# Kernel tuning notes

Measured on AMD Instinct MI355X. Metric: run time of the kernel, lower is better.

Reference implementation:

```python
import jax, jax.numpy as jnp
import numpy as np

B, S, H = 8, 8192, 128          # batch, num_cities, hidden_size
SSIZE, DSIZE = 2, 1             # static (x,y) feats, dynamic feats
STEPS = 20                      # station_num_lim (decode length)


def setup_inputs() -> dict:
    key = jax.random.key(0)
    ks = jax.random.split(key, 16)
    sc = 0.05
    inp = {
        'static': jax.random.normal(ks[0], (B, SSIZE, S), jnp.float32),
        'dynamic': jnp.zeros((B, DSIZE, S), jnp.float32),
        # Encoder convs (kernel_size=1 -> plain linear over channel dim)
        'W_s': jax.random.normal(ks[1], (H, SSIZE), jnp.float32) * sc,
        'b_s': jnp.zeros((H,), jnp.float32),
        'W_d': jax.random.normal(ks[2], (H, DSIZE), jnp.float32) * sc,
        'b_d': jnp.zeros((H,), jnp.float32),
        'W_dec': jax.random.normal(ks[3], (H, SSIZE), jnp.float32) * sc,
        'b_dec': jnp.zeros((H,), jnp.float32),
        # LSTMCell
        'W_ih': jax.random.normal(ks[4], (4 * H, H), jnp.float32) * sc,
        'W_hh': jax.random.normal(ks[5], (4 * H, H), jnp.float32) * sc,
        'b_ih': jnp.zeros((4 * H,), jnp.float32),
        'b_hh': jnp.zeros((4 * H,), jnp.float32),
        # Pointer projections
        'W_ref': jax.random.normal(ks[6], (H, H), jnp.float32) * sc,
        'b_ref': jnp.zeros((H,), jnp.float32),
        'W_pd': jax.random.normal(ks[7], (H, H), jnp.float32) * sc,
        'b_pd': jnp.zeros((H,), jnp.float32),
        'W_q': jax.random.normal(ks[8], (H, H), jnp.float32) * sc,
        'b_q': jnp.zeros((H,), jnp.float32),
        # Additive attention vector (Attention.W, shape (1,H) in torch)
        'W_att': jax.random.normal(ks[9], (H,), jnp.float32) * sc,
        'station_num_lim': STEPS,
    }
    return inp


def reference(static, dynamic, W_s, b_s, W_d, b_d, W_dec, b_dec,
              W_ih, W_hh, b_ih, b_hh, W_ref, b_ref, W_pd, b_pd,
              W_q, b_q, W_att, station_num_lim):
    Bb, _, Ss = static.shape
    Hh = W_s.shape[0]

    # static/dynamic encoders: Conv1d(k=1) == channelwise linear
    static_h = jnp.einsum('bis,hi->bhs', static, W_s) + b_s[None, :, None]
    dynamic_h = jnp.einsum('bis,hi->bhs', dynamic, W_d) + b_d[None, :, None]
    mask = jnp.ones((Bb, Ss), static.dtype)

    def lstm_cell(x, h, c):
        gates = x @ W_ih.T + b_ih + h @ W_hh.T + b_hh
        i, f, g, o = jnp.split(gates, 4, axis=1)
        c2 = jax.nn.sigmoid(f) * c + jax.nn.sigmoid(i) * jnp.tanh(g)
        h2 = jax.nn.sigmoid(o) * jnp.tanh(c2)
        return h2, c2

    def step(carry, _):
        dec_in, hh, cc = carry                      # dec_in: (B, SSIZE)
        dec_hidden = dec_in @ W_dec.T + b_dec       # decoder Encoder, (B, H)
        hh, cc = lstm_cell(dec_hidden, hh, cc)
        # per-step projections (as in the original Pointer.forward)
        ref = jnp.einsum('bhs,gh->bgs', static_h, W_ref) + b_ref[None, :, None]
        dyn = jnp.einsum('bhs,gh->bgs', dynamic_h, W_pd) + b_pd[None, :, None]
        q = hh @ W_q.T + b_q                        # (B, H)
        hidden = jnp.tanh(q[:, :, None] + ref + dyn)  # (B, H, S)
        attns = jnp.einsum('h,bhs->bs', W_att, hidden)
        probs = jax.nn.softmax(attns + mask * 10000.0, axis=1)
        prob = jnp.max(probs, axis=1)               # greedy (eval) select
        ptr = jnp.argmax(probs, axis=1)
        logp = jnp.log(prob)
        dec_in2 = jnp.take_along_axis(static, ptr[:, None, None], axis=2)[:, :, 0]
        return (dec_in2, hh, cc), (ptr, logp)

    dec0 = jnp.zeros((Bb, static.shape[1]), static.dtype)   # x0
    hh0 = jnp.zeros((Bb, Hh), static.dtype)
    cc0 = jnp.zeros((Bb, Hh), static.dtype)
    _, (tour_idx, tour_logp) = jax.lax.scan(
        step, (dec0, hh0, cc0), None, length=station_num_lim)
    return tour_idx.T, tour_logp.T                  # (B, steps), (B, steps)
```

## Files before the change

### kernel.cpp

```cpp
#include <hip/hip_runtime.h>
#include <hip/hip_bf16.h>


#define SS 8192
#define HH 128
#define NB 8

constexpr float kLog2e  = 1.4426950408889634f;
constexpr float kLn2    = 0.6931471805599453f;
constexpr float kBucket = 9.765625e-4f;
constexpr float kBL2e   = kLog2e * 9.765625e-4f;

__device__ __forceinline__ float fsig(float x) {
  return __builtin_amdgcn_rcpf(1.0f + __builtin_amdgcn_exp2f(-x * kLog2e));
}
__device__ __forceinline__ float ftanh(float x) {
  float z = __builtin_amdgcn_exp2f(x * (2.0f * kLog2e));
  return fmaf(-2.0f, __builtin_amdgcn_rcpf(z + 1.0f), 1.0f);
}

__device__ __forceinline__ unsigned long long cld64(const unsigned long long* p) {
  return __hip_atomic_load(p, __ATOMIC_RELAXED, __HIP_MEMORY_SCOPE_AGENT);
}
__device__ __forceinline__ void cst64(unsigned long long* p, unsigned long long v) {
  __hip_atomic_store(p, v, __ATOMIC_RELAXED, __HIP_MEMORY_SCOPE_AGENT);
}

__global__ __launch_bounds__(256, 1)
void drl4_kernel(const float* __restrict__ g_static,
                 const float* __restrict__ g_dynamic,
                 const float* __restrict__ W_s,  const float* __restrict__ b_s,
                 const float* __restrict__ W_d,  const float* __restrict__ b_d,
                 const float* __restrict__ W_dec,const float* __restrict__ b_dec,
                 const float* __restrict__ W_ih, const float* __restrict__ W_hh,
                 const float* __restrict__ b_ih, const float* __restrict__ b_hh,
                 const float* __restrict__ W_ref,const float* __restrict__ b_ref,
                 const float* __restrict__ W_pd, const float* __restrict__ b_pd,
                 const float* __restrict__ W_q,  const float* __restrict__ b_q,
                 const float* __restrict__ W_att,const int* __restrict__ steps_p,
                 float* __restrict__ out,
                 unsigned long long* __restrict__ wrec,
                 unsigned long long* __restrict__ hhrec) {
  const int tid = threadIdx.x;
  const int bid = blockIdx.x;
  const int b   = bid >> 5;
  const int blk = bid & 31;
  const int steps = *steps_p;

  __shared__ float4 s_pack[128];
  __shared__ float  s_ebias[128];
  __shared__ float  s_gb[512];
  __shared__ float  s_g1x[512];
  __shared__ float  s_g1y[512];
  __shared__ float  s_h[128];
  __shared__ __align__(16) float s_qe[128];
  __shared__ float  s_scr[256];

  const int city = blk * 256 + tid;
  const float sx = g_static[(b * 2 + 0) * SS + city];
  const float sy = g_static[(b * 2 + 1) * SS + city];
  const float dd = g_dynamic[b * SS + city];

  const int qrow  = (tid >> 6) * 32 + (tid & 31);
  const int qhalf = (tid >> 5) & 1;
  float wq[64];
  {
    const float* p = W_q + qrow * HH + qhalf * 64;
    #pragma unroll
    for (int j = 0; j < 64; j += 4) {
      float4 v = *(const float4*)(p + j);
      wq[j] = v.x; wq[j+1] = v.y; wq[j+2] = v.z; wq[j+3] = v.w;
    }
  }
  const int ho = tid & 15, hk = tid >> 4;
  float whh[8];
  {
    const float* p = W_hh + (blk * 16 + ho) * HH + hk * 8;
    #pragma unroll
    for (int j = 0; j < 8; j += 4) {
      float4 v = *(const float4*)(p + j);
      whh[j] = v.x; whh[j+1] = v.y; whh[j+2] = v.z; whh[j+3] = v.w;
    }
  }

  for (int g = tid; g < 512; g += 256) {
    const float* wr = W_ih + g * HH;
    float acc = b_ih[g] + b_hh[g];
    float ax = 0.f, ay = 0.f;
    for (int k = 0; k < HH; ++k) {
      float w = wr[k];
      acc = fmaf(w, b_dec[k],      acc);
      ax  = fmaf(w, W_dec[2*k],    ax);
      ay  = fmaf(w, W_dec[2*k+1],  ay);
    }
    s_gb[g] = acc; s_g1x[g] = ax; s_g1y[g] = ay;
  }
  if (tid < 128) {
    float a0 = 0.f, a1 = 0.f, c0 = 0.f, e1 = 0.f, e2 = 0.f;
    const float* wr = W_ref + tid * HH;
    const float* wp = W_pd  + tid * HH;
    for (int k = 0; k < HH; ++k) {
      float w = wr[k], v = wp[k];
      a0 = fmaf(w, W_s[2 * k],     a0);
      a1 = fmaf(w, W_s[2 * k + 1], a1);
      e1 = fmaf(w, b_s[k],         e1);
      c0 = fmaf(v, W_d[k],         c0);
      e2 = fmaf(v, b_d[k],         e2);
    }
    const float sc = 2.0f * kLog2e;
    s_pack[tid]  = make_float4(a0 * sc, a1 * sc, c0 * sc, W_att[tid]);
    s_ebias[tid] = e1 + e2 + b_ref[tid] + b_pd[tid] + b_q[tid];
  }
  float cstate = 0.0f;
  __syncthreads();

  float zb[128], watt[128];
  #pragma unroll
  for (int h = 0; h < 128; ++h) {
    float4 p = s_pack[h];
    zb[h]   = __builtin_amdgcn_exp2f(fmaf(p.x, sx, fmaf(p.y, sy, p.z * dd)));
    watt[h] = p.w;
  }

  const int wv = tid >> 6;
  const int ln = tid & 63;
  for (int t = 0; t < steps; ++t) {
    float hp0 = 0.f, hp1 = 0.f, hp2 = 0.f, hp3 = 0.f;
    float selx = 0.f, sely = 0.f;
    if (t > 0) {
      if (tid < 128) {
        const unsigned expect = (unsigned)t;
        const unsigned long long* wp = wrec + ((t - 1) * 8 + b) * 128;
        const unsigned long long* hp = hhrec + (t & 1) * 4096 + b * 512 + tid;
        unsigned long long w0, w1, h0, h1, h2, h3;
        for (;;) {
          w0 = cld64(wp + ln);       w1 = cld64(wp + 64 + ln);
          h0 = cld64(hp);            h1 = cld64(hp + 128);
          h2 = cld64(hp + 256);      h3 = cld64(hp + 384);
          if (((unsigned)w0 >> 27) == expect && ((unsigned)w1 >> 27) == expect &&
              (unsigned)(h0 >> 32) == expect && (unsigned)(h1 >> 32) == expect &&
              (unsigned)(h2 >> 32) == expect && (unsigned)(h3 >> 32) == expect)
            break;
          __builtin_amdgcn_s_sleep(1);
        }
        unsigned k0 = (unsigned)w0 & 0x07FFFFFFu;
        unsigned k1 = (unsigned)w1 & 0x07FFFFFFu;
        unsigned wmax = k0 > k1 ? k0 : k1;
        #pragma unroll
        for (int k = 1; k < 64; k <<= 1) {
          unsigned o = __shfl_xor(wmax, k);
          wmax = wmax > o ? wmax : o;
        }
        const int ix = 8191 - (int)(wmax & 0x1FFFu);
        hp0 = __uint_as_float((unsigned)h0);
        hp1 = __uint_as_float((unsigned)h1);
        hp2 = __uint_as_float((unsigned)h2);
        hp3 = __uint_as_float((unsigned)h3);
        selx = g_static[(b * 2 + 0) * SS + ix];
        sely = g_static[(b * 2 + 1) * SS + ix];
      }
    }
    if (tid < 128) {
      float gi, gf, gg, go;
      if (t == 0) {
        gi = s_gb[tid];       gf = s_gb[tid + 128];
        gg = s_gb[tid + 256]; go = s_gb[tid + 384];
      } else {
        gi = fmaf(selx, s_g1x[tid],     fmaf(sely, s_g1y[tid],     s_gb[tid]     + hp0));
        gf = fmaf(selx, s_g1x[tid+128], fmaf(sely, s_g1y[tid+128], s_gb[tid+128] + hp1));
        gg = fmaf(selx, s_g1x[tid+256], fmaf(sely, s_g1y[tid+256], s_gb[tid+256] + hp2));
        go = fmaf(selx, s_g1x[tid+384], fmaf(sely, s_g1y[tid+384], s_gb[tid+384] + hp3));
      }
      cstate  = fmaf(fsig(gf), cstate, fsig(gi) * ftanh(gg));
      s_h[tid] = fsig(go) * ftanh(cstate);
    }
    __syncthreads();
    {
      const float* hs = s_h + (qhalf << 6);
      float qa = 0.f;
      #pragma unroll
      for (int u = 0; u < 64; ++u) qa = fmaf(wq[u], hs[u], qa);
      float qo = __shfl_xor(qa, 32);
      if (qhalf == 0) {
        float qe = (qa + qo + s_ebias[qrow]) * (2.0f * kLog2e);
        s_qe[qrow] = __builtin_amdgcn_exp2f(qe);
      }
    }
    {
      const float* hs2 = s_h + hk * 8;
      float pa = 0.f;
      #pragma unroll
      for (int u = 0; u < 8; ++u) pa = fmaf(whh[u], hs2[u], pa);
      s_scr[tid] = pa;
    }
    __syncthreads();
    if (tid < 16) {
      float acc = 0.f;
      #pragma unroll
      for (int j = 0; j < 16; ++j) acc += s_scr[j * 16 + tid];
      cst64(hhrec + ((t + 1) & 1) * 4096 + b * 512 + blk * 16 + tid,
            ((unsigned long long)(unsigned)(t + 1) << 32) |
                __float_as_uint(acc));
    }
    float a0 = 0.f, a1 = 0.f, a2 = 0.f, a3 = 0.f;
    #pragma unroll
    for (int h = 0; h < 128; h += 4) {
      float4 zq = *(const float4*)(s_qe + h);
      float z0 = zb[h+0] * zq.x, z1 = zb[h+1] * zq.y;
      float z2 = zb[h+2] * zq.z, z3 = zb[h+3] * zq.w;
      float r0 = __builtin_amdgcn_rcpf(z0 + 1.0f);
      float r1 = __builtin_amdgcn_rcpf(z1 + 1.0f);
      float r2 = __builtin_amdgcn_rcpf(z2 + 1.0f);
      float r3 = __builtin_amdgcn_rcpf(z3 + 1.0f);
      a0 = fmaf(watt[h+0], fmaf(-2.0f, r0, 1.0f), a0);
      a1 = fmaf(watt[h+1], fmaf(-2.0f, r1, 1.0f), a1);
      a2 = fmaf(watt[h+2], fmaf(-2.0f, r2, 1.0f), a2);
      a3 = fmaf(watt[h+3], fmaf(-2.0f, r3, 1.0f), a3);
    }
    float aq = ((a0 + a1) + (a2 + a3)) + 10000.0f;
    int kk = (int)((aq - 10000.0f) * 1024.0f);
    kk = kk < -8192 ? -8192 : (kk > 8191 ? 8191 : kk);
    unsigned key = ((unsigned)(kk + 8192) << 13) | (unsigned)(8191 - city);
    unsigned wmax = key;
    #pragma unroll
    for (int k = 1; k < 64; k <<= 1) {
      unsigned o = __shfl_xor(wmax, k);
      wmax = wmax > o ? wmax : o;
    }
    float m_w = fmaf((float)((int)((wmax >> 13) & 0x3FFFu) - 8192), kBucket,
                     10000.0f);
    float ee = __builtin_amdgcn_exp2f((aq - m_w) * kLog2e);
    #pragma unroll
    for (int k = 1; k < 64; k <<= 1) ee += __shfl_xor(ee, k);
    if (ln == 0)
      cst64(wrec + (t * 8 + b) * 128 + blk * 4 + wv,
            ((unsigned long long)__float_as_uint(ee) << 32) |
                ((unsigned)(t + 1) << 27) | wmax);
  }
  if (blk == 0) {
    for (int s = wv; s < steps; s += 4) {
      const unsigned long long* wp = wrec + (s * 8 + b) * 128;
      const unsigned expect = (unsigned)(s + 1);
      unsigned long long r0, r1;
      for (;;) {
        r0 = cld64(wp + ln); r1 = cld64(wp + 64 + ln);
        if (((unsigned)r0 >> 27) == expect && ((unsigned)r1 >> 27) == expect)
          break;
        __builtin_amdgcn_s_sleep(1);
      }
      unsigned k0 = (unsigned)r0 & 0x07FFFFFFu;
      unsigned k1 = (unsigned)r1 & 0x07FFFFFFu;
      unsigned wmax = k0 > k1 ? k0 : k1;
      #pragma unroll
      for (int k = 1; k < 64; k <<= 1) {
        unsigned o = __shfl_xor(wmax, k);
        wmax = wmax > o ? wmax : o;
      }
      int K  = (int)((wmax >> 13) & 0x3FFFu) - 8192;
      int i0 = (int)((k0 >> 13) & 0x3FFFu) - 8192;
      int i1 = (int)((k1 >> 13) & 0x3FFFu) - 8192;
      float e0 = __uint_as_float((unsigned)(r0 >> 32));
      float e1 = __uint_as_float((unsigned)(r1 >> 32));
      float term = fmaf(e0, __builtin_amdgcn_exp2f((float)(i0 - K) * kBL2e),
                        e1 * __builtin_amdgcn_exp2f((float)(i1 - K) * kBL2e));
      #pragma unroll
      for (int k = 1; k < 64; k <<= 1) term += __shfl_xor(term, k);
      if (ln == 0) {
        out[b * steps + s] = (float)(8191 - (int)(wmax & 0x1FFFu));
        out[NB * steps + b * steps + s] =
            -__builtin_amdgcn_logf(term) * kLn2;
      }
    }
  }
}

extern "C" void kernel_launch(void* const* d_in, const int* in_sizes, int n_in,
                              void* d_out, int out_size, void* d_ws, size_t ws_size,
                              hipStream_t stream) {
  unsigned long long* wrec  = (unsigned long long*)d_ws;
  unsigned long long* hhrec = (unsigned long long*)((char*)d_ws + 163840);
  drl4_kernel<<<dim3(256), dim3(256), 0, stream>>>(
      (const float*)d_in[0],  (const float*)d_in[1],
      (const float*)d_in[2],  (const float*)d_in[3],
      (const float*)d_in[4],  (const float*)d_in[5],
      (const float*)d_in[6],  (const float*)d_in[7],
      (const float*)d_in[8],  (const float*)d_in[9],
      (const float*)d_in[10], (const float*)d_in[11],
      (const float*)d_in[12], (const float*)d_in[13],
      (const float*)d_in[14], (const float*)d_in[15],
      (const float*)d_in[16], (const float*)d_in[17],
      (const float*)d_in[18], (const int*)d_in[19],
      (float*)d_out, wrec, hhrec);
}
```

Before: 225.4 us.

## Add fast-path sc0 L2 mailbox and per-block argmax key for cross-block step sync

The per-step cross-block exchange is restructured. Each block now reduces its four wave keys to one block key through shared memory, so the critical-path poll reads one record per block instead of two per lane-pair. Key and hidden-state records are written twice, once with sc0 stores to a fast copy and once with agent-scope atomics to a fallback copy. Pollers spin on the fast copy with inline-asm sc0 loads and check the fallback every fourth iteration. Block-to-batch mapping is also interleaved (b = bid & 7). The added block barrier and the non-coherent fast path add risk: a missed update can only be recovered through the slower fallback reads.

```diff
diff --git a/kernel.cpp b/kernel.cpp
--- a/kernel.cpp
+++ b/kernel.cpp
@@ -24,6 +24,10 @@
 }
 __device__ __forceinline__ void cst64(unsigned long long* p, unsigned long long v) {
   __hip_atomic_store(p, v, __ATOMIC_RELAXED, __HIP_MEMORY_SCOPE_AGENT);
+}
+__device__ __forceinline__ void l2st64(unsigned long long* p, unsigned long long v) {
+  asm volatile("global_store_dwordx2 %0, %1, off sc0" :: "v"(p), "v"(v)
+               : "memory");
 }
 
 __global__ __launch_bounds__(256, 1)
@@ -39,12 +43,15 @@
                  const float* __restrict__ W_q,  const float* __restrict__ b_q,
                  const float* __restrict__ W_att,const int* __restrict__ steps_p,
                  float* __restrict__ out,
-                 unsigned long long* __restrict__ wrec,
-                 unsigned long long* __restrict__ hhrec) {
+                 unsigned long long* __restrict__ krecA,
+                 unsigned long long* __restrict__ krecF,
+                 unsigned long long* __restrict__ hhA,
+                 unsigned long long* __restrict__ hhF,
+                 unsigned long long* __restrict__ frec) {
   const int tid = threadIdx.x;
   const int bid = blockIdx.x;
-  const int b   = bid >> 5;
-  const int blk = bid & 31;
+  const int b   = bid & 7;
+  const int blk = bid >> 3;
   const int steps = *steps_p;
 
   __shared__ float4 s_pack[128];
@@ -55,6 +62,7 @@
   __shared__ float  s_h[128];
   __shared__ __align__(16) float s_qe[128];
   __shared__ float  s_scr[256];
+  __shared__ unsigned s_wk[4];
 
   const int city = blk * 256 + tid;
   const float sx = g_static[(b * 2 + 0) * SS + city];
@@ -130,22 +138,44 @@
     if (t > 0) {
       if (tid < 128) {
         const unsigned expect = (unsigned)t;
-        const unsigned long long* wp = wrec + ((t - 1) * 8 + b) * 128;
-        const unsigned long long* hp = hhrec + (t & 1) * 4096 + b * 512 + tid;
-        unsigned long long w0, w1, h0, h1, h2, h3;
+        const int kbase = ((t - 1) & 1) * 256 + b * 32 + (tid & 31);
+        const int hbase = (t & 1) * 4096 + b * 512 + tid;
+        const unsigned long long* kF = krecF + kbase;
+        const unsigned long long* hF = hhF + hbase;
+        const unsigned long long* kA = krecA + kbase;
+        const unsigned long long* hA = hhA + hbase;
+        unsigned long long kv, h0, h1, h2, h3;
+        int it = 0;
         for (;;) {
-          w0 = cld64(wp + ln);       w1 = cld64(wp + 64 + ln);
-          h0 = cld64(hp);            h1 = cld64(hp + 128);
-          h2 = cld64(hp + 256);      h3 = cld64(hp + 384);
-          if (((unsigned)w0 >> 27) == expect && ((unsigned)w1 >> 27) == expect &&
-              (unsigned)(h0 >> 32) == expect && (unsigned)(h1 >> 32) == expect &&
-              (unsigned)(h2 >> 32) == expect && (unsigned)(h3 >> 32) == expect)
-            break;
+          unsigned long long fa, f0, f1, f2, f3;
+          asm volatile(
+              "global_load_dwordx2 %0, %5, off sc0\n\t"
+              "global_load_dwordx2 %1, %6, off sc0\n\t"
+              "global_load_dwordx2 %2, %7, off sc0\n\t"
+              "global_load_dwordx2 %3, %8, off sc0\n\t"
+              "global_load_dwordx2 %4, %9, off sc0\n\t"
+              "s_waitcnt vmcnt(0)"
+              : "=v"(fa), "=v"(f0), "=v"(f1), "=v"(f2), "=v"(f3)
+              : "v"(kF), "v"(hF), "v"(hF + 128), "v"(hF + 256), "v"(hF + 384)
+              : "memory");
+          if ((unsigned)(fa >> 32) == expect && (unsigned)(f0 >> 32) == expect &&
+              (unsigned)(f1 >> 32) == expect && (unsigned)(f2 >> 32) == expect &&
+              (unsigned)(f3 >> 32) == expect) {
+            kv = fa; h0 = f0; h1 = f1; h2 = f2; h3 = f3; break;
+          }
+          if ((++it & 3) == 0) {
+            fa = cld64(kA);
+            f0 = cld64(hA);       f1 = cld64(hA + 128);
+            f2 = cld64(hA + 256); f3 = cld64(hA + 384);
+            if ((unsigned)(fa >> 32) == expect && (unsigned)(f0 >> 32) == expect &&
+                (unsigned)(f1 >> 32) == expect && (unsigned)(f2 >> 32) == expect &&
+                (unsigned)(f3 >> 32) == expect) {
+              kv = fa; h0 = f0; h1 = f1; h2 = f2; h3 = f3; break;
+            }
+          }
           __builtin_amdgcn_s_sleep(1);
         }
-        unsigned k0 = (unsigned)w0 & 0x07FFFFFFu;
-        unsigned k1 = (unsigned)w1 & 0x07FFFFFFu;
-        unsigned wmax = k0 > k1 ? k0 : k1;
+        unsigned wmax = (unsigned)kv;
         #pragma unroll
         for (int k = 1; k < 64; k <<= 1) {
           unsigned o = __shfl_xor(wmax, k);
@@ -198,9 +228,11 @@
       float acc = 0.f;
       #pragma unroll
       for (int j = 0; j < 16; ++j) acc += s_scr[j * 16 + tid];
-      cst64(hhrec + ((t + 1) & 1) * 4096 + b * 512 + blk * 16 + tid,
-            ((unsigned long long)(unsigned)(t + 1) << 32) |
-                __float_as_uint(acc));
+      const int hidx = ((t + 1) & 1) * 4096 + b * 512 + blk * 16 + tid;
+      unsigned long long hv =
+          ((unsigned long long)(unsigned)(t + 1) << 32) | __float_as_uint(acc);
+      l2st64(hhF + hidx, hv);
+      cst64(hhA + hidx, hv);
     }
     float a0 = 0.f, a1 = 0.f, a2 = 0.f, a3 = 0.f;
     #pragma unroll
@@ -227,19 +259,32 @@
       unsigned o = __shfl_xor(wmax, k);
       wmax = wmax > o ? wmax : o;
     }
-    float m_w = fmaf((float)((int)((wmax >> 13) & 0x3FFFu) - 8192), kBucket,
-                     10000.0f);
-    float ee = __builtin_amdgcn_exp2f((aq - m_w) * kLog2e);
+    if (ln == 0) s_wk[wv] = wmax;
+    __syncthreads();
+    unsigned bkey = s_wk[0];
+    bkey = bkey > s_wk[1] ? bkey : s_wk[1];
+    bkey = bkey > s_wk[2] ? bkey : s_wk[2];
+    bkey = bkey > s_wk[3] ? bkey : s_wk[3];
+    if (tid == 0) {
+      const int kidx = (t & 1) * 256 + b * 32 + blk;
+      unsigned long long rv =
+          ((unsigned long long)(unsigned)(t + 1) << 32) | bkey;
+      l2st64(krecF + kidx, rv);
+      cst64(krecA + kidx, rv);
+    }
+    float m = fmaf((float)((int)((bkey >> 13) & 0x3FFFu) - 8192), kBucket,
+                   10000.0f);
+    float ee = __builtin_amdgcn_exp2f((aq - m) * kLog2e);
     #pragma unroll
     for (int k = 1; k < 64; k <<= 1) ee += __shfl_xor(ee, k);
     if (ln == 0)
-      cst64(wrec + (t * 8 + b) * 128 + blk * 4 + wv,
+      cst64(frec + (t * 8 + b) * 128 + blk * 4 + wv,
             ((unsigned long long)__float_as_uint(ee) << 32) |
-                ((unsigned)(t + 1) << 27) | wmax);
+                ((unsigned)(t + 1) << 27) | bkey);
   }
   if (blk == 0) {
     for (int s = wv; s < steps; s += 4) {
-      const unsigned long long* wp = wrec + (s * 8 + b) * 128;
+      const unsigned long long* wp = frec + (s * 8 + b) * 128;
       const unsigned expect = (unsigned)(s + 1);
       unsigned long long r0, r1;
       for (;;) {
@@ -277,8 +322,12 @@
 extern "C" void kernel_launch(void* const* d_in, const int* in_sizes, int n_in,
                               void* d_out, int out_size, void* d_ws, size_t ws_size,
                               hipStream_t stream) {
-  unsigned long long* wrec  = (unsigned long long*)d_ws;
-  unsigned long long* hhrec = (unsigned long long*)((char*)d_ws + 163840);
+  char* ws = (char*)d_ws;
+  unsigned long long* krecA = (unsigned long long*)(ws);
+  unsigned long long* krecF = (unsigned long long*)(ws + 4096);
+  unsigned long long* hhA   = (unsigned long long*)(ws + 8192);
+  unsigned long long* hhF   = (unsigned long long*)(ws + 73728);
+  unsigned long long* frec  = (unsigned long long*)(ws + 139264);
   drl4_kernel<<<dim3(256), dim3(256), 0, stream>>>(
       (const float*)d_in[0],  (const float*)d_in[1],
       (const float*)d_in[2],  (const float*)d_in[3],
@@ -290,5 +339,5 @@
       (const float*)d_in[14], (const float*)d_in[15],
       (const float*)d_in[16], (const float*)d_in[17],
       (const float*)d_in[18], (const int*)d_in[19],
-      (float*)d_out, wrec, hhrec);
-}
+      (float*)d_out, krecA, krecF, hhA, hhF, frec);
+}
```

Result: faster. 216.7 us (-3.8%).

## Publish argmax key before softmax sum to shorten cross-block critical path

Applied to the files above, without the earlier changes.

Splits the per-wave record into an early argmax-key record (double-buffered by step parity), written right after the max reduction, and a later full record holding the exp-sum used only by the final log-prob pass. Blocks waiting for the next step now poll the key record, so the exp and sum reduction no longer sit on the inter-step dependency chain. Also vectorises the setup dot-product loops with float4 loads. This adds an extra global store per wave per step and depends on the parity-based buffer reuse being safe across steps.

```diff
diff --git a/kernel.cpp b/kernel.cpp
--- a/kernel.cpp
+++ b/kernel.cpp
@@ -39,8 +39,9 @@
                  const float* __restrict__ W_q,  const float* __restrict__ b_q,
                  const float* __restrict__ W_att,const int* __restrict__ steps_p,
                  float* __restrict__ out,
-                 unsigned long long* __restrict__ wrec,
-                 unsigned long long* __restrict__ hhrec) {
+                 unsigned long long* __restrict__ krec,
+                 unsigned long long* __restrict__ hhrec,
+                 unsigned long long* __restrict__ frec) {
   const int tid = threadIdx.x;
   const int bid = blockIdx.x;
   const int b   = bid >> 5;
@@ -87,11 +88,15 @@
     const float* wr = W_ih + g * HH;
     float acc = b_ih[g] + b_hh[g];
     float ax = 0.f, ay = 0.f;
-    for (int k = 0; k < HH; ++k) {
-      float w = wr[k];
-      acc = fmaf(w, b_dec[k],      acc);
-      ax  = fmaf(w, W_dec[2*k],    ax);
-      ay  = fmaf(w, W_dec[2*k+1],  ay);
+    for (int k = 0; k < HH; k += 4) {
+      float4 w  = *(const float4*)(wr + k);
+      float4 bd = *(const float4*)(b_dec + k);
+      float4 d0 = *(const float4*)(W_dec + 2 * k);
+      float4 d1 = *(const float4*)(W_dec + 2 * k + 4);
+      acc = fmaf(w.x, bd.x, acc); ax = fmaf(w.x, d0.x, ax); ay = fmaf(w.x, d0.y, ay);
+      acc = fmaf(w.y, bd.y, acc); ax = fmaf(w.y, d0.z, ax); ay = fmaf(w.y, d0.w, ay);
+      acc = fmaf(w.z, bd.z, acc); ax = fmaf(w.z, d1.x, ax); ay = fmaf(w.z, d1.y, ay);
+      acc = fmaf(w.w, bd.w, acc); ax = fmaf(w.w, d1.z, ax); ay = fmaf(w.w, d1.w, ay);
     }
     s_gb[g] = acc; s_g1x[g] = ax; s_g1y[g] = ay;
   }
@@ -99,13 +104,22 @@
     float a0 = 0.f, a1 = 0.f, c0 = 0.f, e1 = 0.f, e2 = 0.f;
     const float* wr = W_ref + tid * HH;
     const float* wp = W_pd  + tid * HH;
-    for (int k = 0; k < HH; ++k) {
-      float w = wr[k], v = wp[k];
-      a0 = fmaf(w, W_s[2 * k],     a0);
-      a1 = fmaf(w, W_s[2 * k + 1], a1);
-      e1 = fmaf(w, b_s[k],         e1);
-      c0 = fmaf(v, W_d[k],         c0);
-      e2 = fmaf(v, b_d[k],         e2);
+    for (int k = 0; k < HH; k += 4) {
+      float4 w  = *(const float4*)(wr + k);
+      float4 v  = *(const float4*)(wp + k);
+      float4 s0 = *(const float4*)(W_s + 2 * k);
+      float4 s1 = *(const float4*)(W_s + 2 * k + 4);
+      float4 bs = *(const float4*)(b_s + k);
+      float4 wd = *(const float4*)(W_d + k);
+      float4 bd = *(const float4*)(b_d + k);
+      a0 = fmaf(w.x, s0.x, a0); a1 = fmaf(w.x, s0.y, a1); e1 = fmaf(w.x, bs.x, e1);
+      c0 = fmaf(v.x, wd.x, c0); e2 = fmaf(v.x, bd.x, e2);
+      a0 = fmaf(w.y, s0.z, a0); a1 = fmaf(w.y, s0.w, a1); e1 = fmaf(w.y, bs.y, e1);
+      c0 = fmaf(v.y, wd.y, c0); e2 = fmaf(v.y, bd.y, e2);
+      a0 = fmaf(w.z, s1.x, a0); a1 = fmaf(w.z, s1.y, a1); e1 = fmaf(w.z, bs.z, e1);
+      c0 = fmaf(v.z, wd.z, c0); e2 = fmaf(v.z, bd.z, e2);
+      a0 = fmaf(w.w, s1.z, a0); a1 = fmaf(w.w, s1.w, a1); e1 = fmaf(w.w, bs.w, e1);
+      c0 = fmaf(v.w, wd.w, c0); e2 = fmaf(v.w, bd.w, e2);
     }
     const float sc = 2.0f * kLog2e;
     s_pack[tid]  = make_float4(a0 * sc, a1 * sc, c0 * sc, W_att[tid]);
@@ -130,22 +144,22 @@
     if (t > 0) {
       if (tid < 128) {
         const unsigned expect = (unsigned)t;
-        const unsigned long long* wp = wrec + ((t - 1) * 8 + b) * 128;
+        const unsigned long long* kp =
+            krec + ((t - 1) & 1) * 1024 + b * 128;
         const unsigned long long* hp = hhrec + (t & 1) * 4096 + b * 512 + tid;
-        unsigned long long w0, w1, h0, h1, h2, h3;
+        unsigned long long k0, k1, h0, h1, h2, h3;
         for (;;) {
-          w0 = cld64(wp + ln);       w1 = cld64(wp + 64 + ln);
+          k0 = cld64(kp + ln);       k1 = cld64(kp + 64 + ln);
           h0 = cld64(hp);            h1 = cld64(hp + 128);
           h2 = cld64(hp + 256);      h3 = cld64(hp + 384);
-          if (((unsigned)w0 >> 27) == expect && ((unsigned)w1 >> 27) == expect &&
+          if ((unsigned)(k0 >> 32) == expect && (unsigned)(k1 >> 32) == expect &&
               (unsigned)(h0 >> 32) == expect && (unsigned)(h1 >> 32) == expect &&
               (unsigned)(h2 >> 32) == expect && (unsigned)(h3 >> 32) == expect)
             break;
           __builtin_amdgcn_s_sleep(1);
         }
-        unsigned k0 = (unsigned)w0 & 0x07FFFFFFu;
-        unsigned k1 = (unsigned)w1 & 0x07FFFFFFu;
-        unsigned wmax = k0 > k1 ? k0 : k1;
+        unsigned u0 = (unsigned)k0, u1 = (unsigned)k1;
+        unsigned wmax = u0 > u1 ? u0 : u1;
         #pragma unroll
         for (int k = 1; k < 64; k <<= 1) {
           unsigned o = __shfl_xor(wmax, k);
@@ -227,19 +241,22 @@
       unsigned o = __shfl_xor(wmax, k);
       wmax = wmax > o ? wmax : o;
     }
+    if (ln == 0)
+      cst64(krec + (t & 1) * 1024 + b * 128 + blk * 4 + wv,
+            ((unsigned long long)(unsigned)(t + 1) << 32) | wmax);
     float m_w = fmaf((float)((int)((wmax >> 13) & 0x3FFFu) - 8192), kBucket,
                      10000.0f);
     float ee = __builtin_amdgcn_exp2f((aq - m_w) * kLog2e);
     #pragma unroll
     for (int k = 1; k < 64; k <<= 1) ee += __shfl_xor(ee, k);
     if (ln == 0)
-      cst64(wrec + (t * 8 + b) * 128 + blk * 4 + wv,
+      cst64(frec + (t * 8 + b) * 128 + blk * 4 + wv,
             ((unsigned long long)__float_as_uint(ee) << 32) |
                 ((unsigned)(t + 1) << 27) | wmax);
   }
   if (blk == 0) {
     for (int s = wv; s < steps; s += 4) {
-      const unsigned long long* wp = wrec + (s * 8 + b) * 128;
+      const unsigned long long* wp = frec + (s * 8 + b) * 128;
       const unsigned expect = (unsigned)(s + 1);
       unsigned long long r0, r1;
       for (;;) {
@@ -277,8 +294,10 @@
 extern "C" void kernel_launch(void* const* d_in, const int* in_sizes, int n_in,
                               void* d_out, int out_size, void* d_ws, size_t ws_size,
                               hipStream_t stream) {
-  unsigned long long* wrec  = (unsigned long long*)d_ws;
-  unsigned long long* hhrec = (unsigned long long*)((char*)d_ws + 163840);
+  char* ws = (char*)d_ws;
+  unsigned long long* krec  = (unsigned long long*)(ws);
+  unsigned long long* hhrec = (unsigned long long*)(ws + 16384);
+  unsigned long long* frec  = (unsigned long long*)(ws + 81920);
   drl4_kernel<<<dim3(256), dim3(256), 0, stream>>>(
       (const float*)d_in[0],  (const float*)d_in[1],
       (const float*)d_in[2],  (const float*)d_in[3],
@@ -290,5 +309,5 @@
       (const float*)d_in[14], (const float*)d_in[15],
       (const float*)d_in[16], (const float*)d_in[17],
       (const float*)d_in[18], (const int*)d_in[19],
-      (float*)d_out, wrec, hhrec);
-}
+      (float*)d_out, krec, hhrec, frec);
+}
```

Result: faster. 209.3 us (-7.1%).
